# Kernel optimization log

Measured on AMD Instinct MI355X. Metric: run time of the kernel, lower is better.

## Reference

```python
import jax, jax.numpy as jnp
import numpy as np

EPS = 1e-4
NEG_BIAS = 0.01


def setup_inputs() -> dict:
    key = jax.random.key(0)
    ks = jax.random.split(key, 9)
    B, L, D_MODEL, HALF = 4, 4096, 2048, 32
    return {
        "u": jax.random.normal(ks[0], (B, L, D_MODEL), dtype=jnp.float32),
        "Lambda_unconstrained_re": jax.random.normal(ks[1], (HALF,), dtype=jnp.float32) * 0.1 - 1.0,
        "Lambda_im": jax.random.normal(ks[2], (HALF,), dtype=jnp.float32) * 3.0,
        "B_re": jax.random.normal(ks[3], (HALF, D_MODEL), dtype=jnp.float32) * 0.02,
        "B_im": jax.random.normal(ks[4], (HALF, D_MODEL), dtype=jnp.float32) * 0.02,
        "C_re": jax.random.normal(ks[5], (D_MODEL, HALF), dtype=jnp.float32) * 0.05,
        "C_im": jax.random.normal(ks[6], (D_MODEL, HALF), dtype=jnp.float32) * 0.05,
        "D": jax.random.normal(ks[7], (D_MODEL,), dtype=jnp.float32) * 0.1,
        "log_Delta": jax.random.uniform(ks[8], (2 * HALF,), minval=-3.0, maxval=-1.0, dtype=jnp.float32),
    }


def reference(u, Lambda_unconstrained_re, Lambda_im, B_re, B_im, C_re, C_im, D, log_Delta):
    half = Lambda_im.shape[0]
    # Constrained continuous-time eigenvalues: Re < 0 via softplus (inverse of init formula)
    lam_re = -(jax.nn.softplus(Lambda_unconstrained_re) + EPS + NEG_BIAS)
    Lam = lam_re + 1j * Lambda_im                      # [half]
    Delta = jnp.exp(log_Delta[:half])                  # per-state timestep
    # ZOH discretization
    Lam_bar = jnp.exp(Lam * Delta)                     # [half]
    B_tilde = (B_re + 1j * B_im).astype(jnp.complex64) # [half, d]
    B_bar = ((Lam_bar - 1.0) / Lam)[:, None] * B_tilde # [half, d]
    # Input projection: Bu[b,l,n]
    Bu = jnp.einsum("bld,nd->bln", u.astype(jnp.complex64), B_bar)
    a = jnp.broadcast_to(Lam_bar, Bu.shape)

    def op(e1, e2):
        a1, b1 = e1
        a2, b2 = e2
        return (a1 * a2, a2 * b1 + b2)

    # Parallel associative scan of x_t = Lam_bar * x_{t-1} + Bu_t along time axis
    _, xs = jax.lax.associative_scan(op, (a, Bu), axis=1)  # [b, l, half]
    C_tilde = (C_re + 1j * C_im).astype(jnp.complex64)     # [d, half]
    # Conjugate symmetry -> 2 * real part, plus skip connection D * u
    y = 2.0 * jnp.real(jnp.einsum("bln,dn->bld", xs, C_tilde)) + D * u
    return y
```

## Files before the change

kernel.cpp:

```cpp
#include <hip/hip_runtime.h>
#include <math.h>

#define M_ROWS 16384
#define DM     2048
#define NJ     64
#define L_SEQ  4096
#define KSPLIT 4

constexpr size_t O_CONSTS = 0;
constexpr size_t O_BBAR   = 128;
constexpr size_t O_CC     = O_BBAR + (size_t)DM * NJ;
constexpr size_t O_BUP    = O_CC + (size_t)NJ * DM;
constexpr size_t O_XS     = O_BUP + (size_t)KSPLIT * M_ROWS * NJ;

__global__ void k_setup(const float* __restrict__ lam_ur, const float* __restrict__ lam_im,
                        const float* __restrict__ log_delta, float* __restrict__ consts) {
  int n = threadIdx.x;
  if (n < 32) {
    float x = lam_ur[n];
    float sp = (x > 20.f) ? x : log1pf(expf(x));
    float lre = -(sp + 1.0e-4f + 0.01f);
    float lim = lam_im[n];
    float dt = expf(log_delta[n]);
    float er = expf(lre * dt);
    float Are = er * cosf(lim * dt);
    float Aim = er * sinf(lim * dt);
    float cr = Are - 1.f, ci = Aim;
    float den = lre * lre + lim * lim;
    float cre = (cr * lre + ci * lim) / den;
    float cim = (ci * lre - cr * lim) / den;
    consts[n] = Are; consts[32 + n] = Aim; consts[64 + n] = cre; consts[96 + n] = cim;
  }
}

__global__ void k_bbar(const float* __restrict__ Bre, const float* __restrict__ Bim,
                       const float* __restrict__ consts, float* __restrict__ bbar_t) {
  int idx = blockIdx.x * 256 + threadIdx.x;
  int d = idx >> 6, j = idx & 63, n = j >> 1;
  float cre = consts[64 + n], cim = consts[96 + n];
  float br = Bre[n * DM + d], bi = Bim[n * DM + d];
  float v = (j & 1) ? (cre * bi + cim * br) : (cre * br - cim * bi);
  bbar_t[idx] = v;
}

__global__ void k_cc(const float* __restrict__ Cre, const float* __restrict__ Cim,
                     float* __restrict__ cc_t) {
  int idx = blockIdx.x * 256 + threadIdx.x;
  int j = idx >> 11, d = idx & 2047, n = j >> 1;
  float v = (j & 1) ? (-2.f * Cim[d * 32 + n]) : (2.f * Cre[d * 32 + n]);
  cc_t[idx] = v;
}

__global__ __launch_bounds__(256) void k_bu(const float* __restrict__ u,
                                            const float* __restrict__ bbar_t,
                                            float* __restrict__ bu_p) {
  __shared__ __align__(16) float As[64][68];
  __shared__ __align__(16) float Bs[64][68];
  const int t = threadIdx.x;
  const int m0 = blockIdx.x * 64;
  const int ks0 = blockIdx.y * (DM / KSPLIT);
  const int q = t & 15;
  const int rb = t >> 4;
  const int tm = t & 15;
  const int tn = t >> 4;
  float acc[4][4] = {};
  for (int kt = 0; kt < 8; ++kt) {
    const int k0 = ks0 + kt * 64;
#pragma unroll
    for (int m = 0; m < 4; ++m) {
      const int row = rb + 16 * m;
      float4 v = *(const float4*)&u[(size_t)(m0 + row) * DM + k0 + 4 * q];
      As[4 * q + 0][row] = v.x;
      As[4 * q + 1][row] = v.y;
      As[4 * q + 2][row] = v.z;
      As[4 * q + 3][row] = v.w;
    }
#pragma unroll
    for (int m = 0; m < 4; ++m) {
      const int kk = rb + 16 * m;
      *(float4*)&Bs[kk][4 * q] = *(const float4*)&bbar_t[(size_t)(k0 + kk) * NJ + 4 * q];
    }
    __syncthreads();
#pragma unroll 8
    for (int k = 0; k < 64; ++k) {
      float4 av = *(const float4*)&As[k][4 * tm];
      float4 bv = *(const float4*)&Bs[k][4 * tn];
      float aa[4] = {av.x, av.y, av.z, av.w};
      float bb[4] = {bv.x, bv.y, bv.z, bv.w};
#pragma unroll
      for (int i = 0; i < 4; ++i)
#pragma unroll
        for (int j = 0; j < 4; ++j)
          acc[i][j] += aa[i] * bb[j];
    }
    __syncthreads();
  }
  float* outp = bu_p + (size_t)blockIdx.y * M_ROWS * NJ;
#pragma unroll
  for (int i = 0; i < 4; ++i) {
    const int row = m0 + 4 * tm + i;
    float4 v = make_float4(acc[i][0], acc[i][1], acc[i][2], acc[i][3]);
    *(float4*)&outp[(size_t)row * NJ + 4 * tn] = v;
  }
}

__global__ __launch_bounds__(256) void k_scan(const float* __restrict__ bu_p,
                                              const float* __restrict__ consts,
                                              float* __restrict__ xs_t) {
  __shared__ float2 sbuf[L_SEQ + 256];
  __shared__ float2 P[256];
  const int n = blockIdx.x;
  const int b = blockIdx.y;
  const int t = threadIdx.x;
  const size_t base = (size_t)b * L_SEQ;
  const float Are = consts[n], Aim = consts[32 + n];
  for (int i = t; i < L_SEQ; i += 256) {
    const size_t row = base + i;
    float re = 0.f, im = 0.f;
#pragma unroll
    for (int s = 0; s < KSPLIT; ++s) {
      float2 v = *(const float2*)&bu_p[((size_t)s * M_ROWS + row) * NJ + 2 * n];
      re += v.x; im += v.y;
    }
    sbuf[i + (i >> 4)] = make_float2(re, im);
  }
  __syncthreads();
  float lre[16], lim[16];
  float xre = 0.f, xim = 0.f;
#pragma unroll
  for (int i = 0; i < 16; ++i) {
    float2 bu = sbuf[17 * t + i];
    float nr = Are * xre - Aim * xim + bu.x;
    float ni = Are * xim + Aim * xre + bu.y;
    xre = nr; xim = ni;
    lre[i] = nr; lim[i] = ni;
  }
  float Mre = Are, Mim = Aim;
#pragma unroll
  for (int k = 0; k < 4; ++k) {
    float nr = Mre * Mre - Mim * Mim;
    float ni = 2.f * Mre * Mim;
    Mre = nr; Mim = ni;
  }
  float pre = xre, pim = xim;
  P[t] = make_float2(pre, pim);
  __syncthreads();
  float msre = Mre, msim = Mim;
  for (int s = 1; s < 256; s <<= 1) {
    float2 prev = (t >= s) ? P[t - s] : make_float2(0.f, 0.f);
    __syncthreads();
    pre += msre * prev.x - msim * prev.y;
    pim += msre * prev.y + msim * prev.x;
    P[t] = make_float2(pre, pim);
    float nr = msre * msre - msim * msim;
    float ni = 2.f * msre * msim;
    msre = nr; msim = ni;
    __syncthreads();
  }
  float2 E = (t == 0) ? make_float2(0.f, 0.f) : P[t - 1];
  float pwre = Are, pwim = Aim;
#pragma unroll
  for (int i = 0; i < 16; ++i) {
    float rre = lre[i] + pwre * E.x - pwim * E.y;
    float rim = lim[i] + pwre * E.y + pwim * E.x;
    sbuf[17 * t + i] = make_float2(rre, rim);
    float nr = pwre * Are - pwim * Aim;
    float ni = pwre * Aim + pwim * Are;
    pwre = nr; pwim = ni;
  }
  __syncthreads();
  float* r0 = xs_t + (size_t)(2 * n) * M_ROWS + base;
  float* r1 = xs_t + (size_t)(2 * n + 1) * M_ROWS + base;
  for (int i = t; i < L_SEQ; i += 256) {
    float2 v = sbuf[i + (i >> 4)];
    r0[i] = v.x;
    r1[i] = v.y;
  }
}

__global__ __launch_bounds__(256) void k_out(const float* __restrict__ xs_t,
                                             const float* __restrict__ cc_t,
                                             const float* __restrict__ u,
                                             const float* __restrict__ Dv,
                                             float* __restrict__ y) {
  __shared__ __align__(16) float As[64][68];
  __shared__ __align__(16) float Bs[64][68];
  const int t = threadIdx.x;
  const int m0 = blockIdx.x * 64;
  const int d0 = blockIdx.y * 64;
  const int q = t & 15;
  const int rb = t >> 4;
#pragma unroll
  for (int m = 0; m < 4; ++m) {
    const int j = rb + 16 * m;
    *(float4*)&As[j][4 * q] = *(const float4*)&xs_t[(size_t)j * M_ROWS + m0 + 4 * q];
    *(float4*)&Bs[j][4 * q] = *(const float4*)&cc_t[(size_t)j * DM + d0 + 4 * q];
  }
  __syncthreads();
  const int tm = t & 15;
  const int tn = t >> 4;
  float acc[4][4] = {};
#pragma unroll 8
  for (int j = 0; j < 64; ++j) {
    float4 av = *(const float4*)&As[j][4 * tm];
    float4 bv = *(const float4*)&Bs[j][4 * tn];
    float aa[4] = {av.x, av.y, av.z, av.w};
    float bb[4] = {bv.x, bv.y, bv.z, bv.w};
#pragma unroll
    for (int i = 0; i < 4; ++i)
#pragma unroll
      for (int jj = 0; jj < 4; ++jj)
        acc[i][jj] += aa[i] * bb[jj];
  }
  float4 dv = *(const float4*)&Dv[d0 + 4 * tn];
  float dd[4] = {dv.x, dv.y, dv.z, dv.w};
#pragma unroll
  for (int i = 0; i < 4; ++i) {
    const size_t row = (size_t)(m0 + 4 * tm + i);
    float4 uv = *(const float4*)&u[row * DM + d0 + 4 * tn];
    float4 o;
    o.x = acc[i][0] + dd[0] * uv.x;
    o.y = acc[i][1] + dd[1] * uv.y;
    o.z = acc[i][2] + dd[2] * uv.z;
    o.w = acc[i][3] + dd[3] * uv.w;
    *(float4*)&y[row * DM + d0 + 4 * tn] = o;
  }
}

extern "C" void kernel_launch(void* const* d_in, const int* in_sizes, int n_in,
                              void* d_out, int out_size, void* d_ws, size_t ws_size,
                              hipStream_t stream) {
  const float* u      = (const float*)d_in[0];
  const float* lam_ur = (const float*)d_in[1];
  const float* lam_im = (const float*)d_in[2];
  const float* B_re   = (const float*)d_in[3];
  const float* B_im   = (const float*)d_in[4];
  const float* C_re   = (const float*)d_in[5];
  const float* C_im   = (const float*)d_in[6];
  const float* Dv     = (const float*)d_in[7];
  const float* log_dt = (const float*)d_in[8];
  float* y  = (float*)d_out;
  float* ws = (float*)d_ws;

  float* consts = ws + O_CONSTS;
  float* bbar_t = ws + O_BBAR;
  float* cc_t   = ws + O_CC;
  float* bu_p   = ws + O_BUP;
  float* xs_t   = ws + O_XS;

  k_setup<<<1, 64, 0, stream>>>(lam_ur, lam_im, log_dt, consts);
  k_bbar<<<(DM * NJ) / 256, 256, 0, stream>>>(B_re, B_im, consts, bbar_t);
  k_cc<<<(NJ * DM) / 256, 256, 0, stream>>>(C_re, C_im, cc_t);
  k_bu<<<dim3(M_ROWS / 64, KSPLIT), 256, 0, stream>>>(u, bbar_t, bu_p);
  k_scan<<<dim3(32, 4), 256, 0, stream>>>(bu_p, consts, xs_t);
  k_out<<<dim3(M_ROWS / 64, DM / 64), 256, 0, stream>>>(xs_t, cc_t, u, Dv, y);
}
```

Measured before the change: 368.4 us.

## Use bf16 MFMA for both projections, fuse prep kernels, drop K-split

Both GEMMs (input projection and output projection) now run on bf16 MFMA 16x16x32 instructions instead of fp32 SIMT FMA. Operands are converted to bf16: u inline, B_bar and C as precomputed tables, and the scan output is stored as packed bf16 in row-major layout. The three setup kernels are fused into a single prep kernel. The scan recomputes the eigenvalues itself, and the K-split partial buffers are removed. The aim is to cut compute and memory traffic, at the cost of bf16 precision in both matmuls, which may exceed tolerance.

```diff
diff --git a/kernel.cpp b/kernel.cpp
--- a/kernel.cpp
+++ b/kernel.cpp
@@ -5,135 +5,119 @@
 #define DM     2048
 #define NJ     64
 #define L_SEQ  4096
-#define KSPLIT 4
-
-constexpr size_t O_CONSTS = 0;
-constexpr size_t O_BBAR   = 128;
-constexpr size_t O_CC     = O_BBAR + (size_t)DM * NJ;
-constexpr size_t O_BUP    = O_CC + (size_t)NJ * DM;
-constexpr size_t O_XS     = O_BUP + (size_t)KSPLIT * M_ROWS * NJ;
-
-__global__ void k_setup(const float* __restrict__ lam_ur, const float* __restrict__ lam_im,
-                        const float* __restrict__ log_delta, float* __restrict__ consts) {
-  int n = threadIdx.x;
-  if (n < 32) {
+
+typedef __bf16 bf16x8 __attribute__((ext_vector_type(8)));
+typedef float  f32x4  __attribute__((ext_vector_type(4)));
+
+constexpr size_t OB_BBART = 0;
+constexpr size_t OB_CCT   = 262144;
+constexpr size_t OB_BU    = 524288;
+constexpr size_t OB_XSB   = 524288 + 4194304;
+
+static __device__ __forceinline__ unsigned short f2bf(float f) {
+  unsigned int u = __float_as_uint(f);
+  u = (u + 0x7fffu + ((u >> 16) & 1u)) >> 16;
+  return (unsigned short)u;
+}
+
+__global__ void k_prep(const float* __restrict__ lam_ur, const float* __restrict__ lam_im,
+                       const float* __restrict__ log_dt,
+                       const float* __restrict__ Bre, const float* __restrict__ Bim,
+                       const float* __restrict__ Cre, const float* __restrict__ Cim,
+                       unsigned short* __restrict__ bbarT, unsigned short* __restrict__ ccT) {
+  const int idx = blockIdx.x * 256 + threadIdx.x;
+  {
+    const int j = idx >> 11, d = idx & 2047, n = j >> 1;
     float x = lam_ur[n];
     float sp = (x > 20.f) ? x : log1pf(expf(x));
     float lre = -(sp + 1.0e-4f + 0.01f);
     float lim = lam_im[n];
-    float dt = expf(log_delta[n]);
+    float dt = expf(log_dt[n]);
     float er = expf(lre * dt);
     float Are = er * cosf(lim * dt);
     float Aim = er * sinf(lim * dt);
-    float cr = Are - 1.f, ci = Aim;
     float den = lre * lre + lim * lim;
-    float cre = (cr * lre + ci * lim) / den;
-    float cim = (ci * lre - cr * lim) / den;
-    consts[n] = Are; consts[32 + n] = Aim; consts[64 + n] = cre; consts[96 + n] = cim;
-  }
-}
-
-__global__ void k_bbar(const float* __restrict__ Bre, const float* __restrict__ Bim,
-                       const float* __restrict__ consts, float* __restrict__ bbar_t) {
-  int idx = blockIdx.x * 256 + threadIdx.x;
-  int d = idx >> 6, j = idx & 63, n = j >> 1;
-  float cre = consts[64 + n], cim = consts[96 + n];
-  float br = Bre[n * DM + d], bi = Bim[n * DM + d];
-  float v = (j & 1) ? (cre * bi + cim * br) : (cre * br - cim * bi);
-  bbar_t[idx] = v;
-}
-
-__global__ void k_cc(const float* __restrict__ Cre, const float* __restrict__ Cim,
-                     float* __restrict__ cc_t) {
-  int idx = blockIdx.x * 256 + threadIdx.x;
-  int j = idx >> 11, d = idx & 2047, n = j >> 1;
-  float v = (j & 1) ? (-2.f * Cim[d * 32 + n]) : (2.f * Cre[d * 32 + n]);
-  cc_t[idx] = v;
+    float cre = ((Are - 1.f) * lre + Aim * lim) / den;
+    float cim = (Aim * lre - (Are - 1.f) * lim) / den;
+    float br = Bre[n * DM + d], bi = Bim[n * DM + d];
+    float v = (j & 1) ? (cre * bi + cim * br) : (cre * br - cim * bi);
+    bbarT[(size_t)j * DM + d] = f2bf(v);
+  }
+  {
+    const int j = idx & 63, d = idx >> 6, n = j >> 1;
+    float v = (j & 1) ? (-2.f * Cim[d * 32 + n]) : (2.f * Cre[d * 32 + n]);
+    ccT[(size_t)d * NJ + j] = f2bf(v);
+  }
 }
 
 __global__ __launch_bounds__(256) void k_bu(const float* __restrict__ u,
-                                            const float* __restrict__ bbar_t,
-                                            float* __restrict__ bu_p) {
-  __shared__ __align__(16) float As[64][68];
-  __shared__ __align__(16) float Bs[64][68];
+                                            const unsigned short* __restrict__ bbarT,
+                                            float* __restrict__ bu) {
   const int t = threadIdx.x;
-  const int m0 = blockIdx.x * 64;
-  const int ks0 = blockIdx.y * (DM / KSPLIT);
-  const int q = t & 15;
-  const int rb = t >> 4;
-  const int tm = t & 15;
-  const int tn = t >> 4;
-  float acc[4][4] = {};
-  for (int kt = 0; kt < 8; ++kt) {
-    const int k0 = ks0 + kt * 64;
-#pragma unroll
-    for (int m = 0; m < 4; ++m) {
-      const int row = rb + 16 * m;
-      float4 v = *(const float4*)&u[(size_t)(m0 + row) * DM + k0 + 4 * q];
-      As[4 * q + 0][row] = v.x;
-      As[4 * q + 1][row] = v.y;
-      As[4 * q + 2][row] = v.z;
-      As[4 * q + 3][row] = v.w;
-    }
-#pragma unroll
-    for (int m = 0; m < 4; ++m) {
-      const int kk = rb + 16 * m;
-      *(float4*)&Bs[kk][4 * q] = *(const float4*)&bbar_t[(size_t)(k0 + kk) * NJ + 4 * q];
-    }
-    __syncthreads();
-#pragma unroll 8
-    for (int k = 0; k < 64; ++k) {
-      float4 av = *(const float4*)&As[k][4 * tm];
-      float4 bv = *(const float4*)&Bs[k][4 * tn];
-      float aa[4] = {av.x, av.y, av.z, av.w};
-      float bb[4] = {bv.x, bv.y, bv.z, bv.w};
-#pragma unroll
-      for (int i = 0; i < 4; ++i)
-#pragma unroll
-        for (int j = 0; j < 4; ++j)
-          acc[i][j] += aa[i] * bb[j];
-    }
-    __syncthreads();
-  }
-  float* outp = bu_p + (size_t)blockIdx.y * M_ROWS * NJ;
+  const int wave = t >> 6, lane = t & 63;
+  const int m0 = blockIdx.x * 32;
+  const int rt = wave & 1;
+  const int ct0 = (wave >> 1) * 2;
+  const int l15 = lane & 15;
+  const int kq = (lane >> 4) * 8;
+  const float* up = u + (size_t)(m0 + rt * 16 + l15) * DM + kq;
+  const bf16x8* b0 = (const bf16x8*)(bbarT + (size_t)(ct0 * 16 + l15) * DM + kq);
+  const bf16x8* b1 = (const bf16x8*)(bbarT + (size_t)(ct0 * 16 + 16 + l15) * DM + kq);
+  f32x4 acc0 = {0.f, 0.f, 0.f, 0.f}, acc1 = {0.f, 0.f, 0.f, 0.f};
+#pragma unroll 4
+  for (int k0 = 0; k0 < DM; k0 += 32) {
+    float4 v0 = *(const float4*)(up + k0);
+    float4 v1 = *(const float4*)(up + k0 + 4);
+    bf16x8 a;
+    a[0] = (__bf16)v0.x; a[1] = (__bf16)v0.y; a[2] = (__bf16)v0.z; a[3] = (__bf16)v0.w;
+    a[4] = (__bf16)v1.x; a[5] = (__bf16)v1.y; a[6] = (__bf16)v1.z; a[7] = (__bf16)v1.w;
+    bf16x8 bb0 = b0[k0 >> 3];
+    bf16x8 bb1 = b1[k0 >> 3];
+    acc0 = __builtin_amdgcn_mfma_f32_16x16x32_bf16(a, bb0, acc0, 0, 0, 0);
+    acc1 = __builtin_amdgcn_mfma_f32_16x16x32_bf16(a, bb1, acc1, 0, 0, 0);
+  }
+  const int col0 = ct0 * 16 + l15;
+  const int orow = m0 + rt * 16 + (lane >> 4) * 4;
 #pragma unroll
   for (int i = 0; i < 4; ++i) {
-    const int row = m0 + 4 * tm + i;
-    float4 v = make_float4(acc[i][0], acc[i][1], acc[i][2], acc[i][3]);
-    *(float4*)&outp[(size_t)row * NJ + 4 * tn] = v;
-  }
-}
-
-__global__ __launch_bounds__(256) void k_scan(const float* __restrict__ bu_p,
-                                              const float* __restrict__ consts,
-                                              float* __restrict__ xs_t) {
+    bu[(size_t)(orow + i) * NJ + col0] = acc0[i];
+    bu[(size_t)(orow + i) * NJ + col0 + 16] = acc1[i];
+  }
+}
+
+__global__ __launch_bounds__(256) void k_scan(const float* __restrict__ bu,
+                                              const float* __restrict__ lam_ur,
+                                              const float* __restrict__ lam_im,
+                                              const float* __restrict__ log_dt,
+                                              unsigned int* __restrict__ xsb32) {
   __shared__ float2 sbuf[L_SEQ + 256];
   __shared__ float2 P[256];
   const int n = blockIdx.x;
   const int b = blockIdx.y;
   const int t = threadIdx.x;
   const size_t base = (size_t)b * L_SEQ;
-  const float Are = consts[n], Aim = consts[32 + n];
+  float x = lam_ur[n];
+  float sp = (x > 20.f) ? x : log1pf(expf(x));
+  float lre = -(sp + 1.0e-4f + 0.01f);
+  float lim = lam_im[n];
+  float dt = expf(log_dt[n]);
+  float er = expf(lre * dt);
+  const float Are = er * cosf(lim * dt);
+  const float Aim = er * sinf(lim * dt);
   for (int i = t; i < L_SEQ; i += 256) {
-    const size_t row = base + i;
-    float re = 0.f, im = 0.f;
-#pragma unroll
-    for (int s = 0; s < KSPLIT; ++s) {
-      float2 v = *(const float2*)&bu_p[((size_t)s * M_ROWS + row) * NJ + 2 * n];
-      re += v.x; im += v.y;
-    }
-    sbuf[i + (i >> 4)] = make_float2(re, im);
+    float2 v = *(const float2*)&bu[(base + i) * NJ + 2 * n];
+    sbuf[i + (i >> 4)] = v;
   }
   __syncthreads();
-  float lre[16], lim[16];
+  float lre16[16], lim16[16];
   float xre = 0.f, xim = 0.f;
 #pragma unroll
   for (int i = 0; i < 16; ++i) {
-    float2 bu = sbuf[17 * t + i];
-    float nr = Are * xre - Aim * xim + bu.x;
-    float ni = Are * xim + Aim * xre + bu.y;
+    float2 buv = sbuf[17 * t + i];
+    float nr = Are * xre - Aim * xim + buv.x;
+    float ni = Are * xim + Aim * xre + buv.y;
     xre = nr; xim = ni;
-    lre[i] = nr; lim[i] = ni;
+    lre16[i] = nr; lim16[i] = ni;
   }
   float Mre = Are, Mim = Aim;
 #pragma unroll
@@ -161,69 +145,55 @@
   float pwre = Are, pwim = Aim;
 #pragma unroll
   for (int i = 0; i < 16; ++i) {
-    float rre = lre[i] + pwre * E.x - pwim * E.y;
-    float rim = lim[i] + pwre * E.y + pwim * E.x;
+    float rre = lre16[i] + pwre * E.x - pwim * E.y;
+    float rim = lim16[i] + pwre * E.y + pwim * E.x;
     sbuf[17 * t + i] = make_float2(rre, rim);
     float nr = pwre * Are - pwim * Aim;
     float ni = pwre * Aim + pwim * Are;
     pwre = nr; pwim = ni;
   }
   __syncthreads();
-  float* r0 = xs_t + (size_t)(2 * n) * M_ROWS + base;
-  float* r1 = xs_t + (size_t)(2 * n + 1) * M_ROWS + base;
   for (int i = t; i < L_SEQ; i += 256) {
     float2 v = sbuf[i + (i >> 4)];
-    r0[i] = v.x;
-    r1[i] = v.y;
-  }
-}
-
-__global__ __launch_bounds__(256) void k_out(const float* __restrict__ xs_t,
-                                             const float* __restrict__ cc_t,
+    xsb32[(base + i) * (NJ / 2) + n] = ((unsigned int)f2bf(v.y) << 16) | f2bf(v.x);
+  }
+}
+
+__global__ __launch_bounds__(256) void k_out(const unsigned short* __restrict__ xsb,
+                                             const unsigned short* __restrict__ ccT,
                                              const float* __restrict__ u,
                                              const float* __restrict__ Dv,
                                              float* __restrict__ y) {
-  __shared__ __align__(16) float As[64][68];
-  __shared__ __align__(16) float Bs[64][68];
   const int t = threadIdx.x;
-  const int m0 = blockIdx.x * 64;
-  const int d0 = blockIdx.y * 64;
-  const int q = t & 15;
-  const int rb = t >> 4;
-#pragma unroll
-  for (int m = 0; m < 4; ++m) {
-    const int j = rb + 16 * m;
-    *(float4*)&As[j][4 * q] = *(const float4*)&xs_t[(size_t)j * M_ROWS + m0 + 4 * q];
-    *(float4*)&Bs[j][4 * q] = *(const float4*)&cc_t[(size_t)j * DM + d0 + 4 * q];
-  }
-  __syncthreads();
-  const int tm = t & 15;
-  const int tn = t >> 4;
-  float acc[4][4] = {};
-#pragma unroll 8
-  for (int j = 0; j < 64; ++j) {
-    float4 av = *(const float4*)&As[j][4 * tm];
-    float4 bv = *(const float4*)&Bs[j][4 * tn];
-    float aa[4] = {av.x, av.y, av.z, av.w};
-    float bb[4] = {bv.x, bv.y, bv.z, bv.w};
-#pragma unroll
-    for (int i = 0; i < 4; ++i)
-#pragma unroll
-      for (int jj = 0; jj < 4; ++jj)
-        acc[i][jj] += aa[i] * bb[jj];
-  }
-  float4 dv = *(const float4*)&Dv[d0 + 4 * tn];
-  float dd[4] = {dv.x, dv.y, dv.z, dv.w};
-#pragma unroll
-  for (int i = 0; i < 4; ++i) {
-    const size_t row = (size_t)(m0 + 4 * tm + i);
-    float4 uv = *(const float4*)&u[row * DM + d0 + 4 * tn];
-    float4 o;
-    o.x = acc[i][0] + dd[0] * uv.x;
-    o.y = acc[i][1] + dd[1] * uv.y;
-    o.z = acc[i][2] + dd[2] * uv.z;
-    o.w = acc[i][3] + dd[3] * uv.w;
-    *(float4*)&y[row * DM + d0 + 4 * tn] = o;
+  const int wave = t >> 6, lane = t & 63;
+  const int m0 = blockIdx.x * 32;
+  const int d0 = blockIdx.y * 128;
+  const int rt = wave & 1;
+  const int ct0 = (wave >> 1) * 4;
+  const int l15 = lane & 15;
+  const int kq = (lane >> 4) * 8;
+  const int row = m0 + rt * 16 + l15;
+  bf16x8 a0 = *(const bf16x8*)(xsb + (size_t)row * NJ + kq);
+  bf16x8 a1 = *(const bf16x8*)(xsb + (size_t)row * NJ + 32 + kq);
+  f32x4 acc[4] = {{0.f,0.f,0.f,0.f},{0.f,0.f,0.f,0.f},{0.f,0.f,0.f,0.f},{0.f,0.f,0.f,0.f}};
+#pragma unroll
+  for (int c = 0; c < 4; ++c) {
+    const int col = d0 + (ct0 + c) * 16 + l15;
+    bf16x8 b0 = *(const bf16x8*)(ccT + (size_t)col * NJ + kq);
+    bf16x8 b1 = *(const bf16x8*)(ccT + (size_t)col * NJ + 32 + kq);
+    acc[c] = __builtin_amdgcn_mfma_f32_16x16x32_bf16(a0, b0, acc[c], 0, 0, 0);
+    acc[c] = __builtin_amdgcn_mfma_f32_16x16x32_bf16(a1, b1, acc[c], 0, 0, 0);
+  }
+  const int orow = m0 + rt * 16 + (lane >> 4) * 4;
+#pragma unroll
+  for (int c = 0; c < 4; ++c) {
+    const int col = d0 + (ct0 + c) * 16 + l15;
+    const float dsc = Dv[col];
+#pragma unroll
+    for (int i = 0; i < 4; ++i) {
+      const size_t off = (size_t)(orow + i) * DM + col;
+      y[off] = acc[c][i] + dsc * u[off];
+    }
   }
 }
 
@@ -239,19 +209,16 @@
   const float* C_im   = (const float*)d_in[6];
   const float* Dv     = (const float*)d_in[7];
   const float* log_dt = (const float*)d_in[8];
-  float* y  = (float*)d_out;
-  float* ws = (float*)d_ws;
-
-  float* consts = ws + O_CONSTS;
-  float* bbar_t = ws + O_BBAR;
-  float* cc_t   = ws + O_CC;
-  float* bu_p   = ws + O_BUP;
-  float* xs_t   = ws + O_XS;
-
-  k_setup<<<1, 64, 0, stream>>>(lam_ur, lam_im, log_dt, consts);
-  k_bbar<<<(DM * NJ) / 256, 256, 0, stream>>>(B_re, B_im, consts, bbar_t);
-  k_cc<<<(NJ * DM) / 256, 256, 0, stream>>>(C_re, C_im, cc_t);
-  k_bu<<<dim3(M_ROWS / 64, KSPLIT), 256, 0, stream>>>(u, bbar_t, bu_p);
-  k_scan<<<dim3(32, 4), 256, 0, stream>>>(bu_p, consts, xs_t);
-  k_out<<<dim3(M_ROWS / 64, DM / 64), 256, 0, stream>>>(xs_t, cc_t, u, Dv, y);
-}
+  float* y = (float*)d_out;
+  char* ws = (char*)d_ws;
+
+  unsigned short* bbarT = (unsigned short*)(ws + OB_BBART);
+  unsigned short* ccT   = (unsigned short*)(ws + OB_CCT);
+  float*          bu    = (float*)(ws + OB_BU);
+  unsigned short* xsb   = (unsigned short*)(ws + OB_XSB);
+
+  k_prep<<<512, 256, 0, stream>>>(lam_ur, lam_im, log_dt, B_re, B_im, C_re, C_im, bbarT, ccT);
+  k_bu<<<M_ROWS / 32, 256, 0, stream>>>(u, bbarT, bu);
+  k_scan<<<dim3(32, 4), 256, 0, stream>>>(bu, lam_ur, lam_im, log_dt, (unsigned int*)xsb);
+  k_out<<<dim3(M_ROWS / 32, DM / 128), 256, 0, stream>>>(xsb, ccT, u, Dv, y);
+}
```

Result: slower. 417.8 us (+13.4%).
